# Kernel optimization log

Measured on AMD Instinct MI355X. Metric: run time of the kernel, lower is better.

## Reference

```python
import jax, jax.numpy as jnp
import numpy as np

N_BUILD = 200000
N_COMM = 10000
E_BUILD = 1200000
E_COMM = 160000
D_B = 64    # building feature dim
D_C = 32    # community feature dim
H = 64      # hidden dim (comm embedding)
D_FUSE = D_B + H  # 128
N_CLS = 2


def gcn(x, src, dst, W, b):
    """PyG-style GCNConv with self-loops and symmetric normalization.
    out_i = sum_{j->i} h_j / sqrt(deg_j * deg_i) + h_i / deg_i + b, h = x @ W.
    deg counts in-edges plus the self-loop."""
    n = x.shape[0]
    h = x @ W                                   # [n, out]
    deg = jnp.ones((n,), x.dtype).at[dst].add(1.0)
    norm = jax.lax.rsqrt(deg)
    msg = h[src] * (norm[src] * norm[dst])[:, None]          # gather + edge weight
    agg = jax.ops.segment_sum(msg, dst, num_segments=n)      # scatter-add
    return agg + h * (1.0 / deg)[:, None] + b


def setup_inputs():
    key = jax.random.key(0)
    ks = jax.random.split(key, 24)
    f32 = jnp.float32

    def glorot(k, shape):
        scale = np.sqrt(2.0 / (shape[0] + shape[1])).astype(np.float32)
        return jax.random.normal(k, shape, dtype=f32) * scale

    inp = {
        "building_features": jax.random.normal(ks[0], (N_BUILD, D_B), dtype=f32),
        "community_features": jax.random.normal(ks[1], (N_COMM, D_C), dtype=f32),
        # GCN weights: comm 32->64->64, attention 128->2, building 128->128->64->2
        "W_c1": glorot(ks[2], (D_C, H)),   "b_c1": jnp.zeros((H,), f32),
        "W_c2": glorot(ks[3], (H, H)),     "b_c2": jnp.zeros((H,), f32),
        "W_att": glorot(ks[4], (D_FUSE, 2)), "b_att": jnp.zeros((2,), f32),
        "W_b1": glorot(ks[5], (D_FUSE, D_FUSE)), "b_b1": jnp.zeros((D_FUSE,), f32),
        "W_b2": glorot(ks[6], (D_FUSE, H)),       "b_b2": jnp.zeros((H,), f32),
        "W_b3": glorot(ks[7], (H, N_CLS)),         "b_b3": jnp.zeros((N_CLS,), f32),
        # edge lists (int) and index maps
        "b_src": jax.random.randint(ks[8], (E_BUILD,), 0, N_BUILD, dtype=jnp.int32),
        "b_dst": jax.random.randint(ks[9], (E_BUILD,), 0, N_BUILD, dtype=jnp.int32),
        "c_src": jax.random.randint(ks[10], (E_COMM,), 0, N_COMM, dtype=jnp.int32),
        "c_dst": jax.random.randint(ks[11], (E_COMM,), 0, N_COMM, dtype=jnp.int32),
        "building_to_comm_mapping": jax.random.randint(ks[12], (N_BUILD,), 0, N_COMM, dtype=jnp.int32),
        # Batch.from_data_list ordering: here identity permutation of buildings
        "local_to_global": jnp.arange(N_BUILD, dtype=jnp.int32),
    }
    return inp


def reference(building_features, community_features,
              W_c1, b_c1, W_c2, b_c2, W_att, b_att,
              W_b1, b_b1, W_b2, b_b2, W_b3, b_b3,
              b_src, b_dst, c_src, c_dst,
              building_to_comm_mapping, local_to_global):
    # Community GNN (dropout is identity in eval)
    comm_x = jax.nn.relu(gcn(community_features, c_src, c_dst, W_c1, b_c1))
    comm_x = jax.nn.relu(gcn(comm_x, c_src, c_dst, W_c2, b_c2))

    # Irregular gather: per-building community embedding
    building_comm = comm_x[building_to_comm_mapping]          # [N_build, H]

    # Feature attention: softmax gate over the two modalities
    logits = jnp.concatenate([building_features, building_comm], axis=1) @ W_att + b_att
    a = jax.nn.softmax(logits, axis=1)                        # [N_build, 2]
    fused = jnp.concatenate([building_features * a[:, 0:1],
                             building_comm * a[:, 1:2]], axis=1)  # [N_build, 128]

    # Batched building GNN over disjoint per-community subgraphs
    local_x = fused[local_to_global]
    x = jax.nn.relu(gcn(local_x, b_src, b_dst, W_b1, b_b1))
    x = jax.nn.relu(gcn(x, b_src, b_dst, W_b2, b_b2))
    x = gcn(x, b_src, b_dst, W_b3, b_b3)                      # [N_build, 2]

    # Scatter back to global order, then log-softmax
    combined = jnp.zeros((building_features.shape[0], N_CLS), x.dtype)
    combined = combined.at[local_to_global].set(x)
    return jax.nn.log_softmax(combined, axis=1)
```

## Files before the change

kernel.cpp:

```cpp
#include <hip/hip_runtime.h>
#include <hip/hip_bf16.h>
#include <math.h>

#define N_BUILD 200000
#define N_COMM  10000
#define E_BUILD 1200000
#define E_COMM  160000
#define NB_B 196
#define NB_C 10
#define CHUNK 2048
#define CB_B ((E_BUILD + CHUNK - 1) / CHUNK)
#define CB_C ((E_COMM  + CHUNK - 1) / CHUNK)

typedef __bf16 bf16x8 __attribute__((ext_vector_type(8)));
typedef float  f32x4  __attribute__((ext_vector_type(4)));

__device__ __forceinline__ unsigned short f2b(float f) {
    unsigned int u = __builtin_bit_cast(unsigned int, f);
    u += 0x7fffu + ((u >> 16) & 1u);
    return (unsigned short)(u >> 16);
}
__device__ __forceinline__ float b2f(unsigned short h) {
    unsigned int u = ((unsigned int)h) << 16;
    return __builtin_bit_cast(float, u);
}
__device__ __forceinline__ unsigned int pk2(float a, float b) {
    return (unsigned int)f2b(a) | ((unsigned int)f2b(b) << 16);
}
__device__ __forceinline__ void up8(uint4 v, float* r) {
    r[0] = b2f((unsigned short)v.x); r[1] = b2f((unsigned short)(v.x >> 16));
    r[2] = b2f((unsigned short)v.y); r[3] = b2f((unsigned short)(v.y >> 16));
    r[4] = b2f((unsigned short)v.z); r[5] = b2f((unsigned short)(v.z >> 16));
    r[6] = b2f((unsigned short)v.w); r[7] = b2f((unsigned short)(v.w >> 16));
}

#define INIT_TOT (N_BUILD + N_COMM + 2 * N_BUILD + N_COMM * 32 + 2048 + 4096 + 16384 + 8192)
__global__ __launch_bounds__(256) void init_k(int* cnt_b, int* cnt_c, float* out,
                                              const float* __restrict__ cF, unsigned short* __restrict__ cFb,
                                              const float* __restrict__ W_c1, unsigned short* __restrict__ Wt_c1,
                                              const float* __restrict__ W_c2, unsigned short* __restrict__ Wt_c2,
                                              const float* __restrict__ W_b1, unsigned short* __restrict__ Wt_b1,
                                              const float* __restrict__ W_b2, unsigned short* __restrict__ Wt_b2) {
    int i = blockIdx.x * blockDim.x + threadIdx.x;
    if (i < N_BUILD) { cnt_b[i] = 0; return; }
    i -= N_BUILD;
    if (i < N_COMM) { cnt_c[i] = 0; return; }
    i -= N_COMM;
    if (i < 2 * N_BUILD) { out[i] = -0.69314718056f; return; }
    i -= 2 * N_BUILD;
    if (i < N_COMM * 32) { cFb[i] = f2b(cF[i]); return; }
    i -= N_COMM * 32;
    if (i < 2048) { Wt_c1[(i % 64) * 32 + i / 64] = f2b(W_c1[i]); return; }
    i -= 2048;
    if (i < 4096) { Wt_c2[(i % 64) * 64 + i / 64] = f2b(W_c2[i]); return; }
    i -= 4096;
    if (i < 16384) { Wt_b1[(i % 128) * 128 + i / 128] = f2b(W_b1[i]); return; }
    i -= 16384;
    if (i < 8192) { Wt_b2[(i % 64) * 128 + i / 64] = f2b(W_b2[i]); }
}


__global__ __launch_bounds__(256) void hist2_k(int* cnt_b, const int* __restrict__ b_dst,
                                               int* cnt_c, const int* __restrict__ c_dst) {
    int i = blockIdx.x * blockDim.x + threadIdx.x;
    if (i < E_BUILD) atomicAdd(&cnt_b[b_dst[i]], 1);
    else if (i < E_BUILD + E_COMM) atomicAdd(&cnt_c[c_dst[i - E_BUILD]], 1);
}

__global__ __launch_bounds__(256) void scan1m_k(const int* __restrict__ cnt_b, int* __restrict__ ex_b, int* __restrict__ bs_b,
                                                const int* __restrict__ cnt_c, int* __restrict__ ex_c, int* __restrict__ bs_c) {
    __shared__ int sdata[256];
    const int tid = threadIdx.x;
    const int* cnt; int* ex; int* bs; int n, blk;
    if ((int)blockIdx.x < NB_B) { cnt = cnt_b; ex = ex_b; bs = bs_b; n = N_BUILD; blk = blockIdx.x; }
    else                        { cnt = cnt_c; ex = ex_c; bs = bs_c; n = N_COMM;  blk = blockIdx.x - NB_B; }
    const int base = blk * 1024 + tid * 4;
    int v[4]; int s = 0;
#pragma unroll
    for (int j = 0; j < 4; ++j) { v[j] = (base + j < n) ? cnt[base + j] : 0; s += v[j]; }
    sdata[tid] = s; __syncthreads();
    for (int off = 1; off < 256; off <<= 1) {
        int t = (tid >= off) ? sdata[tid - off] : 0;
        __syncthreads();
        sdata[tid] += t;
        __syncthreads();
    }
    if (tid == 255) bs[blk] = sdata[255];
    int run = sdata[tid] - s;
#pragma unroll
    for (int j = 0; j < 4; ++j) { if (base + j < n) ex[base + j] = run; run += v[j]; }
}

__global__ __launch_bounds__(256) void scan2m_k(int* bs_b, int* bs_c) {
    __shared__ int sdata[256];
    int* bs = (blockIdx.x == 0) ? bs_b : bs_c;
    int nb  = (blockIdx.x == 0) ? NB_B : NB_C;
    const int tid = threadIdx.x;
    int v = (tid < nb) ? bs[tid] : 0;
    sdata[tid] = v; __syncthreads();
    for (int off = 1; off < 256; off <<= 1) {
        int t = (tid >= off) ? sdata[tid - off] : 0;
        __syncthreads();
        sdata[tid] += t;
        __syncthreads();
    }
    if (tid < nb) bs[tid] = sdata[tid] - v;
}

__global__ __launch_bounds__(256) void finalizem_k(const int* __restrict__ cnt_b, int* rp_b, const int* __restrict__ bo_b,
                                                   int* cur_b, float* di_b,
                                                   const int* __restrict__ cnt_c, int* rp_c, const int* __restrict__ bo_c,
                                                   int* cur_c, float* di_c) {
    int i = blockIdx.x * blockDim.x + threadIdx.x;
    if (i < N_BUILD) {
        int cc = cnt_b[i];
        int r = rp_b[i] + bo_b[i >> 10];
        rp_b[i] = r; cur_b[i] = r; di_b[i] = 1.0f / (float)(cc + 1);
        if (i == 0) { rp_b[N_BUILD] = E_BUILD; rp_c[N_COMM] = E_COMM; }
    } else if (i < N_BUILD + N_COMM) {
        int ic = i - N_BUILD;
        int cc = cnt_c[ic];
        int r = rp_c[ic] + bo_c[ic >> 10];
        rp_c[ic] = r; cur_c[ic] = r; di_c[ic] = 1.0f / (float)(cc + 1);
    }
}

template<int NDIV>
__device__ __forceinline__ void scatter_part(const int* __restrict__ src, const int* __restrict__ dst,
                                             int* cur, const float* __restrict__ di,
                                             int2* __restrict__ cse, int E, int cid, int x) {
    int base = cid * CHUNK + threadIdx.x;
#pragma unroll
    for (int j = 0; j < CHUNK / 256; ++j, base += 256) {
        if (base < E) {
            int d = dst[base];
            if ((unsigned)d / (unsigned)NDIV == (unsigned)x) {
                int s = src[base];
                int pos = atomicAdd(&cur[d], 1);
                cse[pos] = make_int2(s, __float_as_int(sqrtf(di[s] * di[d])));
            }
        }
    }
}

__global__ __launch_bounds__(256) void csr_scatterp_k(const int* __restrict__ b_src, const int* __restrict__ b_dst,
                                                      int* cur_b, const float* __restrict__ di_b, int2* __restrict__ cse_b,
                                                      const int* __restrict__ c_src, const int* __restrict__ c_dst,
                                                      int* cur_c, const float* __restrict__ di_c, int2* __restrict__ cse_c) {
    int bid = blockIdx.x;
    if (bid < 8 * CB_B) {
        scatter_part<N_BUILD / 8>(b_src, b_dst, cur_b, di_b, cse_b, E_BUILD, bid >> 3, bid & 7);
    } else {
        bid -= 8 * CB_B;
        scatter_part<N_COMM / 8>(c_src, c_dst, cur_c, di_c, cse_c, E_COMM, bid >> 3, bid & 7);
    }
}

template<int K, int N, bool GUARD>
__global__ __launch_bounds__(256) void gemm_mfma_k(const unsigned short* __restrict__ X,
                                                   const unsigned short* __restrict__ Wt,
                                                   unsigned short* __restrict__ H, int M) {
    constexpr int GPR = K / 8;
    __shared__ unsigned short sA[64 * K];
    __shared__ unsigned short sB[N * K];
    const int tid  = threadIdx.x;
    const int row0 = blockIdx.x * 64;

    for (int idx = tid; idx < 64 * GPR; idx += 256) {
        int r = idx / GPR, g = idx % GPR;
        uint4 v = make_uint4(0u, 0u, 0u, 0u);
        if (!GUARD || row0 + r < M)
            v = *(const uint4*)&X[(size_t)(row0 + r) * K + g * 8];
        int gs = g ^ (r & (GPR - 1));
        *(uint4*)&sA[r * K + gs * 8] = v;
    }
    for (int idx = tid; idx < N * GPR; idx += 256) {
        int r = idx / GPR, g = idx % GPR;
        uint4 v = *(const uint4*)&Wt[(size_t)r * K + g * 8];
        int gs = g ^ (r & (GPR - 1));
        *(uint4*)&sB[r * K + gs * 8] = v;
    }
    __syncthreads();

    const int wave = tid >> 6, lane = tid & 63;
    const int rA = wave * 16 + (lane & 15);
    const int kg = lane >> 4;

    f32x4 zero = {0.f, 0.f, 0.f, 0.f};
    f32x4 acc[N / 16];
#pragma unroll
    for (int t = 0; t < N / 16; ++t) acc[t] = zero;

#pragma unroll
    for (int ks = 0; ks < K / 32; ++ks) {
        int gA = (ks * 4 + kg) ^ (rA & (GPR - 1));
        bf16x8 a = *(const bf16x8*)&sA[rA * K + gA * 8];
#pragma unroll
        for (int t = 0; t < N / 16; ++t) {
            int rB = t * 16 + (lane & 15);
            int gB = (ks * 4 + kg) ^ (rB & (GPR - 1));
            bf16x8 b = *(const bf16x8*)&sB[rB * K + gB * 8];
            acc[t] = __builtin_amdgcn_mfma_f32_16x16x32_bf16(a, b, acc[t], 0, 0, 0);
        }
    }

    const int crow = wave * 16 + (lane >> 4) * 4;
    const int ccol = lane & 15;
#pragma unroll
    for (int t = 0; t < N / 16; ++t) {
#pragma unroll
        for (int j = 0; j < 4; ++j) {
            int r = row0 + crow + j;
            if (!GUARD || r < M)
                H[(size_t)r * N + t * 16 + ccol] = f2b(acc[t][j]);
        }
    }
}

__global__ __launch_bounds__(256) void gemm_att_k(const float* __restrict__ bF,
                                                  const unsigned short* __restrict__ cx,
                                                  const int* __restrict__ map,
                                                  const int* __restrict__ l2g,
                                                  const float* __restrict__ Watt,
                                                  const float* __restrict__ batt,
                                                  const unsigned short* __restrict__ Wt,
                                                  unsigned short* __restrict__ H) {
    constexpr int K = 128, N = 128, GPR = 16;
    __shared__ unsigned short sA[64 * K];
    __shared__ unsigned short sB[N * K];
    __shared__ float sWt[256];
    const int tid = threadIdx.x;
    const int row0 = blockIdx.x * 64;
    sWt[tid] = Watt[tid];
    for (int idx = tid; idx < N * GPR; idx += 256) {
        int r = idx / GPR, g = idx % GPR;
        uint4 v = *(const uint4*)&Wt[(size_t)r * K + g * 8];
        int gs = g ^ (r & (GPR - 1));
        *(uint4*)&sB[r * K + gs * 8] = v;
    }
    __syncthreads();
    {
        const int r = tid >> 2, j = tid & 3;
        const int g = l2g[row0 + r];
        float vals[32];
        if (j < 2) {
            const float* f1 = &bF[(size_t)g * 64 + j * 32];
#pragma unroll
            for (int t = 0; t < 8; ++t) {
                float4 v = *(const float4*)&f1[t * 4];
                vals[t*4+0]=v.x; vals[t*4+1]=v.y; vals[t*4+2]=v.z; vals[t*4+3]=v.w;
            }
        } else {
            const unsigned short* f2 = &cx[(size_t)map[g] * 64 + (j & 1) * 32];
#pragma unroll
            for (int t = 0; t < 4; ++t) {
                uint4 u = *(const uint4*)&f2[t * 8];
                up8(u, &vals[t * 8]);
            }
        }
        float l0 = 0.f, l1 = 0.f;
        const int ch0 = j * 32;
#pragma unroll
        for (int t = 0; t < 32; ++t) {
            l0 = fmaf(vals[t], sWt[(ch0 + t) * 2 + 0], l0);
            l1 = fmaf(vals[t], sWt[(ch0 + t) * 2 + 1], l1);
        }
        l0 += __shfl_xor(l0, 1, 4); l0 += __shfl_xor(l0, 2, 4);
        l1 += __shfl_xor(l1, 1, 4); l1 += __shfl_xor(l1, 2, 4);
        l0 += batt[0]; l1 += batt[1];
        float mm = fmaxf(l0, l1);
        float e0 = __expf(l0 - mm), e1 = __expf(l1 - mm);
        float a = ((j < 2) ? e0 : e1) / (e0 + e1);
#pragma unroll
        for (int t = 0; t < 4; ++t) {
            uint4 o;
            o.x = pk2(vals[t*8+0]*a, vals[t*8+1]*a);
            o.y = pk2(vals[t*8+2]*a, vals[t*8+3]*a);
            o.z = pk2(vals[t*8+4]*a, vals[t*8+5]*a);
            o.w = pk2(vals[t*8+6]*a, vals[t*8+7]*a);
            int gi = j * 4 + t;
            int gs = gi ^ (r & (GPR - 1));
            *(uint4*)&sA[r * K + gs * 8] = o;
        }
    }
    __syncthreads();
    const int wave = tid >> 6, lane = tid & 63;
    const int rA = wave * 16 + (lane & 15);
    const int kg = lane >> 4;
    f32x4 zero = {0.f, 0.f, 0.f, 0.f};
    f32x4 acc[8];
#pragma unroll
    for (int t = 0; t < 8; ++t) acc[t] = zero;
#pragma unroll
    for (int ks = 0; ks < 4; ++ks) {
        int gA = (ks * 4 + kg) ^ (rA & 15);
        bf16x8 a = *(const bf16x8*)&sA[rA * K + gA * 8];
#pragma unroll
        for (int t = 0; t < 8; ++t) {
            int rB = t * 16 + (lane & 15);
            int gB = (ks * 4 + kg) ^ (rB & 15);
            bf16x8 b = *(const bf16x8*)&sB[rB * K + gB * 8];
            acc[t] = __builtin_amdgcn_mfma_f32_16x16x32_bf16(a, b, acc[t], 0, 0, 0);
        }
    }
    const int crow = wave * 16 + (lane >> 4) * 4;
    const int ccol = lane & 15;
#pragma unroll
    for (int t = 0; t < 8; ++t)
#pragma unroll
        for (int jj = 0; jj < 4; ++jj)
            H[(size_t)(row0 + crow + jj) * N + t * 16 + ccol] = f2b(acc[t][jj]);
}

__global__ __launch_bounds__(256) void gather_gemm_k(const int* __restrict__ rowptr,
                                                     const int2* __restrict__ cse,
                                                     const unsigned short* __restrict__ h,
                                                     const float* __restrict__ dinv,
                                                     const float* __restrict__ bias,
                                                     const unsigned short* __restrict__ Wt,
                                                     unsigned short* __restrict__ H) {
    constexpr int K = 128, N = 64, GPR = 16;
    __shared__ unsigned short sA[64 * K];
    __shared__ unsigned short sB[N * K];
    const int tid = threadIdx.x;
    const int row0 = blockIdx.x * 64;
    for (int idx = tid; idx < N * GPR; idx += 256) {
        int r = idx / GPR, g = idx % GPR;
        uint4 v = *(const uint4*)&Wt[(size_t)r * K + g * 8];
        int gs = g ^ (r & (GPR - 1));
        *(uint4*)&sB[r * K + gs * 8] = v;
    }
    const int lane = tid & 63;
    const int wave = tid >> 6;
    const int slot = lane >> 4;
    const int c = (lane & 15) * 8;
#pragma unroll
    for (int sb = 0; sb < 4; ++sb) {
        const int r = wave * 16 + sb * 4 + slot;
        const int node = row0 + r;
        int beg = rowptr[node], end = rowptr[node + 1];
        uint4 hv = *(const uint4*)&h[(size_t)node * K + c];
        float iv = dinv[node];
        float4 bb0 = *(const float4*)&bias[c];
        float4 bb1 = *(const float4*)&bias[c + 4];
        float acc[8];
#pragma unroll
        for (int i = 0; i < 8; ++i) acc[i] = 0.f;
        for (int p = beg; p < end; p += 8) {
            int2 q[8]; uint4 v[8];
#pragma unroll
            for (int t = 0; t < 8; ++t) { int e = p + t; q[t] = cse[e < end ? e : 0]; }
#pragma unroll
            for (int t = 0; t < 8; ++t) v[t] = *(const uint4*)&h[(size_t)q[t].x * K + c];
#pragma unroll
            for (int t = 0; t < 8; ++t) {
                float w = (p + t < end) ? __int_as_float(q[t].y) : 0.f;
                float rr[8]; up8(v[t], rr);
#pragma unroll
                for (int i = 0; i < 8; ++i) acc[i] = fmaf(rr[i], w, acc[i]);
            }
        }
        float hr[8]; up8(hv, hr);
        float o[8];
        o[0] = fmaf(hr[0], iv, acc[0]) + bb0.x; o[1] = fmaf(hr[1], iv, acc[1]) + bb0.y;
        o[2] = fmaf(hr[2], iv, acc[2]) + bb0.z; o[3] = fmaf(hr[3], iv, acc[3]) + bb0.w;
        o[4] = fmaf(hr[4], iv, acc[4]) + bb1.x; o[5] = fmaf(hr[5], iv, acc[5]) + bb1.y;
        o[6] = fmaf(hr[6], iv, acc[6]) + bb1.z; o[7] = fmaf(hr[7], iv, acc[7]) + bb1.w;
#pragma unroll
        for (int i = 0; i < 8; ++i) o[i] = fmaxf(o[i], 0.f);
        uint4 ov;
        ov.x = pk2(o[0], o[1]); ov.y = pk2(o[2], o[3]);
        ov.z = pk2(o[4], o[5]); ov.w = pk2(o[6], o[7]);
        const int g = lane & 15;
        const int gs = g ^ (r & (GPR - 1));
        *(uint4*)&sA[r * K + gs * 8] = ov;
    }
    __syncthreads();
    const int rA = wave * 16 + (lane & 15);
    const int kg = lane >> 4;
    f32x4 zero = {0.f, 0.f, 0.f, 0.f};
    f32x4 acc[4];
#pragma unroll
    for (int t = 0; t < 4; ++t) acc[t] = zero;
#pragma unroll
    for (int ks = 0; ks < 4; ++ks) {
        int gA = (ks * 4 + kg) ^ (rA & (GPR - 1));
        bf16x8 a = *(const bf16x8*)&sA[rA * K + gA * 8];
#pragma unroll
        for (int t = 0; t < 4; ++t) {
            int rB = t * 16 + (lane & 15);
            int gB = (ks * 4 + kg) ^ (rB & (GPR - 1));
            bf16x8 b = *(const bf16x8*)&sB[rB * K + gB * 8];
            acc[t] = __builtin_amdgcn_mfma_f32_16x16x32_bf16(a, b, acc[t], 0, 0, 0);
        }
    }
    const int crow = wave * 16 + (lane >> 4) * 4;
    const int ccol = lane & 15;
#pragma unroll
    for (int t = 0; t < 4; ++t)
#pragma unroll
        for (int jj = 0; jj < 4; ++jj)
            H[(size_t)(row0 + crow + jj) * N + t * 16 + ccol] = f2b(acc[t][jj]);
}

template<int F, bool RELU>
__global__ __launch_bounds__(256) void gatherF_k(const int* __restrict__ rowptr,
                                                 const int2* __restrict__ cse,
                                                 const unsigned short* __restrict__ h,
                                                 const float* __restrict__ dinv,
                                                 const float* __restrict__ bias,
                                                 unsigned short* __restrict__ out, int nGrp) {
    constexpr int LPN = F / 8;
    constexpr int NPW = 64 / LPN;
    int wid = (blockIdx.x * blockDim.x + threadIdx.x) >> 6;
    int lane = threadIdx.x & 63;
    if (wid >= nGrp) return;
    int node = wid * NPW + lane / LPN;
    int c = (lane % LPN) * 8;
    int beg = rowptr[node], end = rowptr[node + 1];
    uint4 hv = *(const uint4*)&h[(size_t)node * F + c];
    float iv = dinv[node];
    float4 bb0 = *(const float4*)&bias[c];
    float4 bb1 = *(const float4*)&bias[c + 4];
    float acc[8];
#pragma unroll
    for (int i = 0; i < 8; ++i) acc[i] = 0.f;
    for (int p = beg; p < end; p += 8) {
        int2 q[8]; uint4 v[8];
#pragma unroll
        for (int t = 0; t < 8; ++t) { int e = p + t; q[t] = cse[e < end ? e : 0]; }
#pragma unroll
        for (int t = 0; t < 8; ++t) v[t] = *(const uint4*)&h[(size_t)q[t].x * F + c];
#pragma unroll
        for (int t = 0; t < 8; ++t) {
            float w = (p + t < end) ? __int_as_float(q[t].y) : 0.f;
            float r[8]; up8(v[t], r);
#pragma unroll
            for (int i = 0; i < 8; ++i) acc[i] = fmaf(r[i], w, acc[i]);
        }
    }
    float hr[8]; up8(hv, hr);
    float o[8];
    o[0] = fmaf(hr[0], iv, acc[0]) + bb0.x; o[1] = fmaf(hr[1], iv, acc[1]) + bb0.y;
    o[2] = fmaf(hr[2], iv, acc[2]) + bb0.z; o[3] = fmaf(hr[3], iv, acc[3]) + bb0.w;
    o[4] = fmaf(hr[4], iv, acc[4]) + bb1.x; o[5] = fmaf(hr[5], iv, acc[5]) + bb1.y;
    o[6] = fmaf(hr[6], iv, acc[6]) + bb1.z; o[7] = fmaf(hr[7], iv, acc[7]) + bb1.w;
    if (RELU) {
#pragma unroll
        for (int i = 0; i < 8; ++i) o[i] = fmaxf(o[i], 0.f);
    }
    uint4 ov;
    ov.x = pk2(o[0], o[1]); ov.y = pk2(o[2], o[3]);
    ov.z = pk2(o[4], o[5]); ov.w = pk2(o[6], o[7]);
    *(uint4*)&out[(size_t)node * F + c] = ov;
}

__global__ __launch_bounds__(256) void gather64_dot_k(const int* __restrict__ rowptr,
                                                      const int2* __restrict__ cse,
                                                      const unsigned short* __restrict__ h,
                                                      const float* __restrict__ dinv,
                                                      const float* __restrict__ bias,
                                                      const float* __restrict__ W3,
                                                      float* __restrict__ Dh, int nOct) {
    int wid = (blockIdx.x * blockDim.x + threadIdx.x) >> 6;
    int lane = threadIdx.x & 63;
    if (wid >= nOct) return;
    int node = wid * 8 + (lane >> 3);
    int sl = lane & 7, c = sl * 8;
    int beg = rowptr[node], end = rowptr[node + 1];
    uint4 hv = *(const uint4*)&h[(size_t)node * 64 + c];
    float iv = dinv[node];
    float4 bb0 = *(const float4*)&bias[c];
    float4 bb1 = *(const float4*)&bias[c + 4];
    float4 w4[4];
#pragma unroll
    for (int i = 0; i < 4; ++i) w4[i] = *(const float4*)&W3[c * 2 + i * 4];
    float acc[8];
#pragma unroll
    for (int i = 0; i < 8; ++i) acc[i] = 0.f;
    for (int p = beg; p < end; p += 8) {
        int2 q[8]; uint4 v[8];
#pragma unroll
        for (int t = 0; t < 8; ++t) { int e = p + t; q[t] = cse[e < end ? e : 0]; }
#pragma unroll
        for (int t = 0; t < 8; ++t) v[t] = *(const uint4*)&h[(size_t)q[t].x * 64 + c];
#pragma unroll
        for (int t = 0; t < 8; ++t) {
            float w = (p + t < end) ? __int_as_float(q[t].y) : 0.f;
            float r[8]; up8(v[t], r);
#pragma unroll
            for (int i = 0; i < 8; ++i) acc[i] = fmaf(r[i], w, acc[i]);
        }
    }
    float hr[8]; up8(hv, hr);
    float o[8];
    o[0] = fmaf(hr[0], iv, acc[0]) + bb0.x; o[1] = fmaf(hr[1], iv, acc[1]) + bb0.y;
    o[2] = fmaf(hr[2], iv, acc[2]) + bb0.z; o[3] = fmaf(hr[3], iv, acc[3]) + bb0.w;
    o[4] = fmaf(hr[4], iv, acc[4]) + bb1.x; o[5] = fmaf(hr[5], iv, acc[5]) + bb1.y;
    o[6] = fmaf(hr[6], iv, acc[6]) + bb1.z; o[7] = fmaf(hr[7], iv, acc[7]) + bb1.w;
#pragma unroll
    for (int i = 0; i < 8; ++i) o[i] = fmaxf(o[i], 0.f);
    float d0 = 0.f, d1 = 0.f;
#pragma unroll
    for (int i = 0; i < 4; ++i) {
        d0 = fmaf(o[2*i],   w4[i].x, d0); d0 = fmaf(o[2*i+1], w4[i].z, d0);
        d1 = fmaf(o[2*i],   w4[i].y, d1); d1 = fmaf(o[2*i+1], w4[i].w, d1);
    }
#pragma unroll
    for (int m = 1; m < 8; m <<= 1) {
        d0 += __shfl_xor(d0, m, 8);
        d1 += __shfl_xor(d1, m, 8);
    }
    if (sl == 0) {
        Dh[2 * (size_t)node + 0] = d0;
        Dh[2 * (size_t)node + 1] = d1;
    }
}

__global__ __launch_bounds__(256) void gather2_logsm_k(const int* __restrict__ rowptr,
                                                       const int2* __restrict__ cse,
                                                       const float* __restrict__ h2,
                                                       const float* __restrict__ dinv,
                                                       const float* __restrict__ bias,
                                                       const int* __restrict__ l2g,
                                                       float* __restrict__ out, int n) {
    int i = blockIdx.x * blockDim.x + threadIdx.x;
    if (i >= n) return;
    int beg = rowptr[i], end = rowptr[i + 1];
    float2 hv = *(const float2*)&h2[2 * (size_t)i];
    float iv = dinv[i];
    float a = 0.f, b = 0.f;
    for (int p = beg; p < end; p += 8) {
        int2 q[8]; float2 v[8];
#pragma unroll
        for (int t = 0; t < 8; ++t) { int e = p + t; q[t] = cse[e < end ? e : 0]; }
#pragma unroll
        for (int t = 0; t < 8; ++t) v[t] = *(const float2*)&h2[2 * (size_t)q[t].x];
#pragma unroll
        for (int t = 0; t < 8; ++t) {
            float w = (p + t < end) ? __int_as_float(q[t].y) : 0.f;
            a = fmaf(v[t].x, w, a);
            b = fmaf(v[t].y, w, b);
        }
    }
    a = fmaf(hv.x, iv, a) + bias[0];
    b = fmaf(hv.y, iv, b) + bias[1];
    float m = fmaxf(a, b);
    float ls = m + logf(__expf(a - m) + __expf(b - m));
    int g = l2g[i];
    out[2 * (size_t)g + 0] = a - ls;
    out[2 * (size_t)g + 1] = b - ls;
}


static inline dim3 g1(long long n, int tpb = 256) { return dim3((unsigned)((n + tpb - 1) / tpb)); }

extern "C" void kernel_launch(void* const* d_in, const int* in_sizes, int n_in,
                              void* d_out, int out_size, void* d_ws, size_t ws_size,
                              hipStream_t stream) {
    const float* bF   = (const float*)d_in[0];
    const float* cF   = (const float*)d_in[1];
    const float* W_c1 = (const float*)d_in[2];
    const float* b_c1 = (const float*)d_in[3];
    const float* W_c2 = (const float*)d_in[4];
    const float* b_c2 = (const float*)d_in[5];
    const float* W_at = (const float*)d_in[6];
    const float* b_at = (const float*)d_in[7];
    const float* W_b1 = (const float*)d_in[8];
    const float* b_b1 = (const float*)d_in[9];
    const float* W_b2 = (const float*)d_in[10];
    const float* b_b2 = (const float*)d_in[11];
    const float* W_b3 = (const float*)d_in[12];
    const float* b_b3 = (const float*)d_in[13];
    const int* b_src = (const int*)d_in[14];
    const int* b_dst = (const int*)d_in[15];
    const int* c_src = (const int*)d_in[16];
    const int* c_dst = (const int*)d_in[17];
    const int* map   = (const int*)d_in[18];
    const int* l2g   = (const int*)d_in[19];
    float* out = (float*)d_out;

    char* p = (char*)d_ws;
    auto alloc = [&](size_t bytes) { char* q = p; p += (bytes + 15) & ~(size_t)15; return q; };
    int*   cnt_b    = (int*)  alloc(N_BUILD * 4);
    int*   rowptr_b = (int*)  alloc((N_BUILD + 4) * 4);
    int*   cursor_b = (int*)  alloc(N_BUILD * 4);
    int*   bsum_b   = (int*)  alloc(256 * 4);
    int*   cnt_c    = (int*)  alloc(N_COMM * 4);
    int*   rowptr_c = (int*)  alloc((N_COMM + 4) * 4);
    int*   cursor_c = (int*)  alloc(N_COMM * 4);
    int*   bsum_c   = (int*)  alloc(256 * 4);
    int2*  cse_b    = (int2*) alloc((size_t)E_BUILD * 8);
    int2*  cse_c    = (int2*) alloc((size_t)E_COMM * 8);
    float* dinv_b   = (float*)alloc(N_BUILD * 4);
    float* dinv_c   = (float*)alloc(N_COMM * 4);
    unsigned short* cFb    = (unsigned short*)alloc((size_t)N_COMM * 32 * 2);
    unsigned short* Wt_c1  = (unsigned short*)alloc(64 * 32 * 2);
    unsigned short* Wt_c2  = (unsigned short*)alloc(64 * 64 * 2);
    unsigned short* Wt_b1  = (unsigned short*)alloc(128 * 128 * 2);
    unsigned short* Wt_b2  = (unsigned short*)alloc(64 * 128 * 2);
    unsigned short* ch_bf  = (unsigned short*)alloc((size_t)N_COMM * 64 * 2);
    unsigned short* cx1_bf = (unsigned short*)alloc((size_t)N_COMM * 64 * 2);
    unsigned short* cx2_bf = (unsigned short*)alloc((size_t)N_COMM * 64 * 2);
    unsigned short* A_bf   = (unsigned short*)alloc((size_t)N_BUILD * 128 * 2);
    unsigned short* B_bf   = (unsigned short*)alloc((size_t)N_BUILD * 128 * 2);
    float* Dh = (float*)alloc((size_t)N_BUILD * 2 * 4);

    init_k<<<g1(INIT_TOT), 256, 0, stream>>>(cnt_b, cnt_c, out,
                                             cF, cFb, W_c1, Wt_c1, W_c2, Wt_c2, W_b1, Wt_b1, W_b2, Wt_b2);
    hist2_k<<<g1(E_BUILD + E_COMM), 256, 0, stream>>>(cnt_b, b_dst, cnt_c, c_dst);
    scan1m_k<<<NB_B + NB_C, 256, 0, stream>>>(cnt_b, rowptr_b, bsum_b, cnt_c, rowptr_c, bsum_c);
    scan2m_k<<<2, 256, 0, stream>>>(bsum_b, bsum_c);
    finalizem_k<<<g1(N_BUILD + N_COMM), 256, 0, stream>>>(cnt_b, rowptr_b, bsum_b, cursor_b, dinv_b,
                                                          cnt_c, rowptr_c, bsum_c, cursor_c, dinv_c);
    csr_scatterp_k<<<8 * (CB_B + CB_C), 256, 0, stream>>>(b_src, b_dst, cursor_b, dinv_b, cse_b,
                                                          c_src, c_dst, cursor_c, dinv_c, cse_c);

    gemm_mfma_k<32, 64, true><<<dim3((N_COMM + 63) / 64), 256, 0, stream>>>(cFb, Wt_c1, ch_bf, N_COMM);
    gatherF_k<64, true><<<g1((long long)(N_COMM / 8) * 64), 256, 0, stream>>>(rowptr_c, cse_c, ch_bf, dinv_c, b_c1, cx1_bf, N_COMM / 8);

    gemm_mfma_k<64, 64, true><<<dim3((N_COMM + 63) / 64), 256, 0, stream>>>(cx1_bf, Wt_c2, ch_bf, N_COMM);
    gatherF_k<64, true><<<g1((long long)(N_COMM / 8) * 64), 256, 0, stream>>>(rowptr_c, cse_c, ch_bf, dinv_c, b_c2, cx2_bf, N_COMM / 8);

    gemm_att_k<<<dim3(N_BUILD / 64), 256, 0, stream>>>(bF, cx2_bf, map, l2g, W_at, b_at, Wt_b1, B_bf);

    gather_gemm_k<<<dim3(N_BUILD / 64), 256, 0, stream>>>(rowptr_b, cse_b, B_bf, dinv_b, b_b1, Wt_b2, A_bf);

    gather64_dot_k<<<g1((long long)(N_BUILD / 8) * 64), 256, 0, stream>>>(rowptr_b, cse_b, A_bf, dinv_b, b_b2, W_b3, Dh, N_BUILD / 8);

    gather2_logsm_k<<<g1(N_BUILD), 256, 0, stream>>>(rowptr_b, cse_b, Dh, dinv_b, b_b3, l2g, out, N_BUILD);
}
```

Before: 321.6 us.

## Store CSR source indices only and recompute edge weights from per-node rsqrt degrees

The CSR edge array shrinks from (src, weight) int2 pairs to plain int source indices. Each gather kernel now recomputes the edge weight as sqrt(dinv[src]) * sqrt(dinv[dst]), using a new per-node sqrt-degree array filled in the finalize kernel. This halves the edge stream written by the scatter kernel and read by each of the five aggregation passes, and it drops the dinv[s] lookups from the scatter. In exchange, every edge needs an extra random 4-byte gather of sqd[src] in each aggregation pass.

```diff
diff --git a/kernel.cpp b/kernel.cpp
--- a/kernel.cpp
+++ b/kernel.cpp
@@ -108,51 +108,51 @@
 }
 
 __global__ __launch_bounds__(256) void finalizem_k(const int* __restrict__ cnt_b, int* rp_b, const int* __restrict__ bo_b,
-                                                   int* cur_b, float* di_b,
+                                                   int* cur_b, float* di_b, float* sq_b,
                                                    const int* __restrict__ cnt_c, int* rp_c, const int* __restrict__ bo_c,
-                                                   int* cur_c, float* di_c) {
+                                                   int* cur_c, float* di_c, float* sq_c) {
     int i = blockIdx.x * blockDim.x + threadIdx.x;
     if (i < N_BUILD) {
         int cc = cnt_b[i];
         int r = rp_b[i] + bo_b[i >> 10];
-        rp_b[i] = r; cur_b[i] = r; di_b[i] = 1.0f / (float)(cc + 1);
+        float di = 1.0f / (float)(cc + 1);
+        rp_b[i] = r; cur_b[i] = r; di_b[i] = di; sq_b[i] = sqrtf(di);
         if (i == 0) { rp_b[N_BUILD] = E_BUILD; rp_c[N_COMM] = E_COMM; }
     } else if (i < N_BUILD + N_COMM) {
         int ic = i - N_BUILD;
         int cc = cnt_c[ic];
         int r = rp_c[ic] + bo_c[ic >> 10];
-        rp_c[ic] = r; cur_c[ic] = r; di_c[ic] = 1.0f / (float)(cc + 1);
+        float di = 1.0f / (float)(cc + 1);
+        rp_c[ic] = r; cur_c[ic] = r; di_c[ic] = di; sq_c[ic] = sqrtf(di);
     }
 }
 
 template<int NDIV>
 __device__ __forceinline__ void scatter_part(const int* __restrict__ src, const int* __restrict__ dst,
-                                             int* cur, const float* __restrict__ di,
-                                             int2* __restrict__ cse, int E, int cid, int x) {
+                                             int* cur, int* __restrict__ csrc, int E, int cid, int x) {
     int base = cid * CHUNK + threadIdx.x;
 #pragma unroll
     for (int j = 0; j < CHUNK / 256; ++j, base += 256) {
         if (base < E) {
             int d = dst[base];
             if ((unsigned)d / (unsigned)NDIV == (unsigned)x) {
-                int s = src[base];
                 int pos = atomicAdd(&cur[d], 1);
-                cse[pos] = make_int2(s, __float_as_int(sqrtf(di[s] * di[d])));
+                csrc[pos] = src[base];
             }
         }
     }
 }
 
 __global__ __launch_bounds__(256) void csr_scatterp_k(const int* __restrict__ b_src, const int* __restrict__ b_dst,
-                                                      int* cur_b, const float* __restrict__ di_b, int2* __restrict__ cse_b,
+                                                      int* cur_b, int* __restrict__ csrc_b,
                                                       const int* __restrict__ c_src, const int* __restrict__ c_dst,
-                                                      int* cur_c, const float* __restrict__ di_c, int2* __restrict__ cse_c) {
+                                                      int* cur_c, int* __restrict__ csrc_c) {
     int bid = blockIdx.x;
     if (bid < 8 * CB_B) {
-        scatter_part<N_BUILD / 8>(b_src, b_dst, cur_b, di_b, cse_b, E_BUILD, bid >> 3, bid & 7);
+        scatter_part<N_BUILD / 8>(b_src, b_dst, cur_b, csrc_b, E_BUILD, bid >> 3, bid & 7);
     } else {
         bid -= 8 * CB_B;
-        scatter_part<N_COMM / 8>(c_src, c_dst, cur_c, di_c, cse_c, E_COMM, bid >> 3, bid & 7);
+        scatter_part<N_COMM / 8>(c_src, c_dst, cur_c, csrc_c, E_COMM, bid >> 3, bid & 7);
     }
 }
 
@@ -313,7 +313,8 @@
 }
 
 __global__ __launch_bounds__(256) void gather_gemm_k(const int* __restrict__ rowptr,
-                                                     const int2* __restrict__ cse,
+                                                     const int* __restrict__ csrc,
+                                                     const float* __restrict__ sqd,
                                                      const unsigned short* __restrict__ h,
                                                      const float* __restrict__ dinv,
                                                      const float* __restrict__ bias,
@@ -341,20 +342,23 @@
         int beg = rowptr[node], end = rowptr[node + 1];
         uint4 hv = *(const uint4*)&h[(size_t)node * K + c];
         float iv = dinv[node];
+        float sqn = sqd[node];
         float4 bb0 = *(const float4*)&bias[c];
         float4 bb1 = *(const float4*)&bias[c + 4];
         float acc[8];
 #pragma unroll
         for (int i = 0; i < 8; ++i) acc[i] = 0.f;
         for (int p = beg; p < end; p += 8) {
-            int2 q[8]; uint4 v[8];
-#pragma unroll
-            for (int t = 0; t < 8; ++t) { int e = p + t; q[t] = cse[e < end ? e : 0]; }
-#pragma unroll
-            for (int t = 0; t < 8; ++t) v[t] = *(const uint4*)&h[(size_t)q[t].x * K + c];
+            int q[8]; uint4 v[8]; float sq[8];
+#pragma unroll
+            for (int t = 0; t < 8; ++t) { int e = p + t; q[t] = csrc[e < end ? e : 0]; }
+#pragma unroll
+            for (int t = 0; t < 8; ++t) v[t] = *(const uint4*)&h[(size_t)q[t] * K + c];
+#pragma unroll
+            for (int t = 0; t < 8; ++t) sq[t] = sqd[q[t]];
 #pragma unroll
             for (int t = 0; t < 8; ++t) {
-                float w = (p + t < end) ? __int_as_float(q[t].y) : 0.f;
+                float w = (p + t < end) ? sq[t] * sqn : 0.f;
                 float rr[8]; up8(v[t], rr);
 #pragma unroll
                 for (int i = 0; i < 8; ++i) acc[i] = fmaf(rr[i], w, acc[i]);
@@ -400,12 +404,13 @@
     for (int t = 0; t < 4; ++t)
 #pragma unroll
         for (int jj = 0; jj < 4; ++jj)
-            H[(size_t)(row0 + crow + jj) * N + t * 16 + ccol] = f2b(acc[t][jj]);
+            H[(size_t)(row0 + crow + jj) * 64 + t * 16 + ccol] = f2b(acc[t][jj]);
 }
 
 template<int F, bool RELU>
 __global__ __launch_bounds__(256) void gatherF_k(const int* __restrict__ rowptr,
-                                                 const int2* __restrict__ cse,
+                                                 const int* __restrict__ csrc,
+                                                 const float* __restrict__ sqd,
                                                  const unsigned short* __restrict__ h,
                                                  const float* __restrict__ dinv,
                                                  const float* __restrict__ bias,
@@ -420,20 +425,23 @@
     int beg = rowptr[node], end = rowptr[node + 1];
     uint4 hv = *(const uint4*)&h[(size_t)node * F + c];
     float iv = dinv[node];
+    float sqn = sqd[node];
     float4 bb0 = *(const float4*)&bias[c];
     float4 bb1 = *(const float4*)&bias[c + 4];
     float acc[8];
 #pragma unroll
     for (int i = 0; i < 8; ++i) acc[i] = 0.f;
     for (int p = beg; p < end; p += 8) {
-        int2 q[8]; uint4 v[8];
-#pragma unroll
-        for (int t = 0; t < 8; ++t) { int e = p + t; q[t] = cse[e < end ? e : 0]; }
-#pragma unroll
-        for (int t = 0; t < 8; ++t) v[t] = *(const uint4*)&h[(size_t)q[t].x * F + c];
+        int q[8]; uint4 v[8]; float sq[8];
+#pragma unroll
+        for (int t = 0; t < 8; ++t) { int e = p + t; q[t] = csrc[e < end ? e : 0]; }
+#pragma unroll
+        for (int t = 0; t < 8; ++t) v[t] = *(const uint4*)&h[(size_t)q[t] * F + c];
+#pragma unroll
+        for (int t = 0; t < 8; ++t) sq[t] = sqd[q[t]];
 #pragma unroll
         for (int t = 0; t < 8; ++t) {
-            float w = (p + t < end) ? __int_as_float(q[t].y) : 0.f;
+            float w = (p + t < end) ? sq[t] * sqn : 0.f;
             float r[8]; up8(v[t], r);
 #pragma unroll
             for (int i = 0; i < 8; ++i) acc[i] = fmaf(r[i], w, acc[i]);
@@ -456,7 +464,8 @@
 }
 
 __global__ __launch_bounds__(256) void gather64_dot_k(const int* __restrict__ rowptr,
-                                                      const int2* __restrict__ cse,
+                                                      const int* __restrict__ csrc,
+                                                      const float* __restrict__ sqd,
                                                       const unsigned short* __restrict__ h,
                                                       const float* __restrict__ dinv,
                                                       const float* __restrict__ bias,
@@ -470,6 +479,7 @@
     int beg = rowptr[node], end = rowptr[node + 1];
     uint4 hv = *(const uint4*)&h[(size_t)node * 64 + c];
     float iv = dinv[node];
+    float sqn = sqd[node];
     float4 bb0 = *(const float4*)&bias[c];
     float4 bb1 = *(const float4*)&bias[c + 4];
     float4 w4[4];
@@ -479,14 +489,16 @@
 #pragma unroll
     for (int i = 0; i < 8; ++i) acc[i] = 0.f;
     for (int p = beg; p < end; p += 8) {
-        int2 q[8]; uint4 v[8];
-#pragma unroll
-        for (int t = 0; t < 8; ++t) { int e = p + t; q[t] = cse[e < end ? e : 0]; }
-#pragma unroll
-        for (int t = 0; t < 8; ++t) v[t] = *(const uint4*)&h[(size_t)q[t].x * 64 + c];
+        int q[8]; uint4 v[8]; float sq[8];
+#pragma unroll
+        for (int t = 0; t < 8; ++t) { int e = p + t; q[t] = csrc[e < end ? e : 0]; }
+#pragma unroll
+        for (int t = 0; t < 8; ++t) v[t] = *(const uint4*)&h[(size_t)q[t] * 64 + c];
+#pragma unroll
+        for (int t = 0; t < 8; ++t) sq[t] = sqd[q[t]];
 #pragma unroll
         for (int t = 0; t < 8; ++t) {
-            float w = (p + t < end) ? __int_as_float(q[t].y) : 0.f;
+            float w = (p + t < end) ? sq[t] * sqn : 0.f;
             float r[8]; up8(v[t], r);
 #pragma unroll
             for (int i = 0; i < 8; ++i) acc[i] = fmaf(r[i], w, acc[i]);
@@ -518,7 +530,8 @@
 }
 
 __global__ __launch_bounds__(256) void gather2_logsm_k(const int* __restrict__ rowptr,
-                                                       const int2* __restrict__ cse,
+                                                       const int* __restrict__ csrc,
+                                                       const float* __restrict__ sqd,
                                                        const float* __restrict__ h2,
                                                        const float* __restrict__ dinv,
                                                        const float* __restrict__ bias,
@@ -529,16 +542,19 @@
     int beg = rowptr[i], end = rowptr[i + 1];
     float2 hv = *(const float2*)&h2[2 * (size_t)i];
     float iv = dinv[i];
+    float sqn = sqd[i];
     float a = 0.f, b = 0.f;
     for (int p = beg; p < end; p += 8) {
-        int2 q[8]; float2 v[8];
-#pragma unroll
-        for (int t = 0; t < 8; ++t) { int e = p + t; q[t] = cse[e < end ? e : 0]; }
-#pragma unroll
-        for (int t = 0; t < 8; ++t) v[t] = *(const float2*)&h2[2 * (size_t)q[t].x];
+        int q[8]; float2 v[8]; float sq[8];
+#pragma unroll
+        for (int t = 0; t < 8; ++t) { int e = p + t; q[t] = csrc[e < end ? e : 0]; }
+#pragma unroll
+        for (int t = 0; t < 8; ++t) v[t] = *(const float2*)&h2[2 * (size_t)q[t]];
+#pragma unroll
+        for (int t = 0; t < 8; ++t) sq[t] = sqd[q[t]];
 #pragma unroll
         for (int t = 0; t < 8; ++t) {
-            float w = (p + t < end) ? __int_as_float(q[t].y) : 0.f;
+            float w = (p + t < end) ? sq[t] * sqn : 0.f;
             a = fmaf(v[t].x, w, a);
             b = fmaf(v[t].y, w, b);
         }
@@ -590,10 +606,12 @@
     int*   rowptr_c = (int*)  alloc((N_COMM + 4) * 4);
     int*   cursor_c = (int*)  alloc(N_COMM * 4);
     int*   bsum_c   = (int*)  alloc(256 * 4);
-    int2*  cse_b    = (int2*) alloc((size_t)E_BUILD * 8);
-    int2*  cse_c    = (int2*) alloc((size_t)E_COMM * 8);
+    int*   csrc_b   = (int*)  alloc((size_t)E_BUILD * 4);
+    int*   csrc_c   = (int*)  alloc((size_t)E_COMM * 4);
     float* dinv_b   = (float*)alloc(N_BUILD * 4);
+    float* sqd_b    = (float*)alloc(N_BUILD * 4);
     float* dinv_c   = (float*)alloc(N_COMM * 4);
+    float* sqd_c    = (float*)alloc(N_COMM * 4);
     unsigned short* cFb    = (unsigned short*)alloc((size_t)N_COMM * 32 * 2);
     unsigned short* Wt_c1  = (unsigned short*)alloc(64 * 32 * 2);
     unsigned short* Wt_c2  = (unsigned short*)alloc(64 * 64 * 2);
@@ -611,22 +629,22 @@
     hist2_k<<<g1(E_BUILD + E_COMM), 256, 0, stream>>>(cnt_b, b_dst, cnt_c, c_dst);
     scan1m_k<<<NB_B + NB_C, 256, 0, stream>>>(cnt_b, rowptr_b, bsum_b, cnt_c, rowptr_c, bsum_c);
     scan2m_k<<<2, 256, 0, stream>>>(bsum_b, bsum_c);
-    finalizem_k<<<g1(N_BUILD + N_COMM), 256, 0, stream>>>(cnt_b, rowptr_b, bsum_b, cursor_b, dinv_b,
-                                                          cnt_c, rowptr_c, bsum_c, cursor_c, dinv_c);
-    csr_scatterp_k<<<8 * (CB_B + CB_C), 256, 0, stream>>>(b_src, b_dst, cursor_b, dinv_b, cse_b,
-                                                          c_src, c_dst, cursor_c, dinv_c, cse_c);
+    finalizem_k<<<g1(N_BUILD + N_COMM), 256, 0, stream>>>(cnt_b, rowptr_b, bsum_b, cursor_b, dinv_b, sqd_b,
+                                                          cnt_c, rowptr_c, bsum_c, cursor_c, dinv_c, sqd_c);
+    csr_scatterp_k<<<8 * (CB_B + CB_C), 256, 0, stream>>>(b_src, b_dst, cursor_b, csrc_b,
+                                                          c_src, c_dst, cursor_c, csrc_c);
 
     gemm_mfma_k<32, 64, true><<<dim3((N_COMM + 63) / 64), 256, 0, stream>>>(cFb, Wt_c1, ch_bf, N_COMM);
-    gatherF_k<64, true><<<g1((long long)(N_COMM / 8) * 64), 256, 0, stream>>>(rowptr_c, cse_c, ch_bf, dinv_c, b_c1, cx1_bf, N_COMM / 8);
+    gatherF_k<64, true><<<g1((long long)(N_COMM / 8) * 64), 256, 0, stream>>>(rowptr_c, csrc_c, sqd_c, ch_bf, dinv_c, b_c1, cx1_bf, N_COMM / 8);
 
     gemm_mfma_k<64, 64, true><<<dim3((N_COMM + 63) / 64), 256, 0, stream>>>(cx1_bf, Wt_c2, ch_bf, N_COMM);
-    gatherF_k<64, true><<<g1((long long)(N_COMM / 8) * 64), 256, 0, stream>>>(rowptr_c, cse_c, ch_bf, dinv_c, b_c2, cx2_bf, N_COMM / 8);
+    gatherF_k<64, true><<<g1((long long)(N_COMM / 8) * 64), 256, 0, stream>>>(rowptr_c, csrc_c, sqd_c, ch_bf, dinv_c, b_c2, cx2_bf, N_COMM / 8);
 
     gemm_att_k<<<dim3(N_BUILD / 64), 256, 0, stream>>>(bF, cx2_bf, map, l2g, W_at, b_at, Wt_b1, B_bf);
 
-    gather_gemm_k<<<dim3(N_BUILD / 64), 256, 0, stream>>>(rowptr_b, cse_b, B_bf, dinv_b, b_b1, Wt_b2, A_bf);
-
-    gather64_dot_k<<<g1((long long)(N_BUILD / 8) * 64), 256, 0, stream>>>(rowptr_b, cse_b, A_bf, dinv_b, b_b2, W_b3, Dh, N_BUILD / 8);
-
-    gather2_logsm_k<<<g1(N_BUILD), 256, 0, stream>>>(rowptr_b, cse_b, Dh, dinv_b, b_b3, l2g, out, N_BUILD);
-}
+    gather_gemm_k<<<dim3(N_BUILD / 64), 256, 0, stream>>>(rowptr_b, csrc_b, sqd_b, B_bf, dinv_b, b_b1, Wt_b2, A_bf);
+
+    gather64_dot_k<<<g1((long long)(N_BUILD / 8) * 64), 256, 0, stream>>>(rowptr_b, csrc_b, sqd_b, A_bf, dinv_b, b_b2, W_b3, Dh, N_BUILD / 8);
+
+    gather2_logsm_k<<<g1(N_BUILD), 256, 0, stream>>>(rowptr_b, csrc_b, sqd_b, Dh, dinv_b, b_b3, l2g, out, N_BUILD);
+}
```

Result: slower. 337.1 us (+4.8%).
